# Performance work log

Hardware: AMD Instinct MI355X
Metric: run time of the kernel (lower is better)

## Reference

```python
import jax, jax.numpy as jnp
import numpy as np

BS, EP = 32, 32
N_AGENTS, N_ATOM, EMBED = 8, 51, 32
STATE_DIM, HYP = 128, 64
V_MIN, V_MAX = -10.0, 10.0


def proj(support, probs, v_min, v_max, n_atom):
    # C51 categorical projection of (support, probs) onto the fixed atom grid
    # linspace(v_min, v_max, n_atom). support/probs: [..., M] -> [..., n_atom]
    support, probs = jnp.broadcast_arrays(support, probs)
    delta = (v_max - v_min) / (n_atom - 1)
    b = (jnp.clip(support, v_min, v_max) - v_min) / delta
    l = jnp.floor(b)
    u = jnp.ceil(b)
    eq = (u == l).astype(probs.dtype)  # support exactly on an atom -> all mass to l
    ml = probs * (u - b + eq)
    mu = probs * (b - l)
    shp = probs.shape
    n = int(np.prod(shp[:-1]))
    m = shp[-1]
    rows = jnp.arange(n)[:, None]
    out = jnp.zeros((n, n_atom), probs.dtype)
    out = out.at[rows, l.astype(jnp.int32).reshape(n, m)].add(ml.reshape(n, m))
    out = out.at[rows, u.astype(jnp.int32).reshape(n, m)].add(mu.reshape(n, m))
    return out.reshape(shp[:-1] + (n_atom,))


def bconv(p, q):
    # Full 1D convolution of per-row categorical pmfs (sum of two random vars).
    # p: [N, L], q: [N, M] -> [N, L+M-1], via grouped conv (one group per row).
    N, L = p.shape
    M = q.shape[-1]
    out = jax.lax.conv_general_dilated(
        p[None], jnp.flip(q, -1)[:, None, :],
        window_strides=(1,), padding=[(M - 1, M - 1)],
        feature_group_count=N, dimension_numbers=('NCW', 'OIW', 'NCW'))
    return out[0]


def mlp2(x, w1, b1, w2, b2):
    return jax.nn.relu(x @ w1.T + b1) @ w2.T + b2


def setup_inputs():
    key = jax.random.key(0)
    ks = jax.random.split(key, 20)
    def p(k, shape, s=0.05):
        return jax.random.normal(k, shape, dtype=jnp.float32) * s
    aq = jax.random.uniform(ks[0], (BS, EP, N_AGENTS, N_ATOM), dtype=jnp.float32)
    aq = aq / jnp.sum(aq, -1, keepdims=True)  # valid categorical distributions
    return {
        'agent_qs_distri': aq,
        'states': p(ks[1], (BS, EP, STATE_DIM), 1.0),
        'hw1_w1': p(ks[2], (HYP, STATE_DIM)), 'hw1_b1': p(ks[3], (HYP,)),
        'hw1_w2': p(ks[4], (EMBED * N_AGENTS, HYP)), 'hw1_b2': p(ks[5], (EMBED * N_AGENTS,)),
        'hb1_w': p(ks[6], (EMBED, STATE_DIM)), 'hb1_b': p(ks[7], (EMBED,)),
        'hwf_w1': p(ks[8], (HYP, STATE_DIM)), 'hwf_b1': p(ks[9], (HYP,)),
        'hwf_w2': p(ks[10], (EMBED, HYP)), 'hwf_b2': p(ks[11], (EMBED,)),
        'v_w1': p(ks[12], (EMBED, STATE_DIM)), 'v_b1': p(ks[13], (EMBED,)),
        'v_w2': p(ks[14], (1, EMBED)), 'v_b2': p(ks[15], (1,)),
    }


def reference(agent_qs_distri, states, hw1_w1, hw1_b1, hw1_w2, hw1_b2,
              hb1_w, hb1_b, hwf_w1, hwf_b1, hwf_w2, hwf_b2,
              v_w1, v_b1, v_w2, v_b2):
    bs, ep, n_agents, n_atom = agent_qs_distri.shape
    s = states.reshape(-1, STATE_DIM)
    atoms = jnp.linspace(V_MIN, V_MAX, n_atom).astype(jnp.float32)  # [A]

    w1 = jnp.abs(mlp2(s, hw1_w1, hw1_b1, hw1_w2, hw1_b2)).reshape(bs, ep, EMBED, n_agents)
    b1 = (s @ hb1_w.T + hb1_b).reshape(bs, ep, EMBED)

    # stage 1: scale each agent's support by w1[..., k, i], project back onto atoms
    sup1 = atoms * w1[..., None]                                       # [bs,ep,E,Na,A]
    aw = proj(sup1, agent_qs_distri[:, :, None], V_MIN, V_MAX, n_atom)  # [bs,ep,E,Na,A]
    awf = aw.reshape(-1, n_agents, n_atom)                              # [bs*ep*E,Na,A]
    q = awf[:, 0]
    for i in range(1, n_agents):
        q = bconv(q, awf[:, i])                                         # [.., Na*A-Na+1]
    L1 = n_agents * n_atom - n_agents + 1
    sup = jnp.linspace(n_agents * V_MIN, n_agents * V_MAX, L1).astype(jnp.float32)
    sup = jax.nn.elu(sup + b1[..., None])                               # [bs,ep,E,L1]
    x = proj(sup, q.reshape(bs, ep, EMBED, L1), V_MIN, V_MAX, n_atom)   # [bs,ep,E,A]

    # stage 2: hyper_w_final scaling, convolve across embed dim, add V(s)
    wf = jnp.abs(mlp2(s, hwf_w1, hwf_b1, hwf_w2, hwf_b2)).reshape(bs, ep, EMBED)
    xw = proj(atoms * wf[..., None], x, V_MIN, V_MAX, n_atom)           # [bs,ep,E,A]
    xwf = xw.reshape(-1, EMBED, n_atom)
    q = xwf[:, 0]
    for i in range(1, EMBED):
        q = bconv(q, xwf[:, i])                                         # [bs*ep, E*A-E+1]
    L2 = EMBED * n_atom - EMBED + 1
    v = mlp2(s, v_w1, v_b1, v_w2, v_b2).reshape(bs, ep, 1)
    sup2 = jnp.linspace(EMBED * V_MIN, EMBED * V_MAX, L2).astype(jnp.float32) + v
    return proj(sup2, q.reshape(bs, ep, L2), V_MIN, V_MAX, n_atom)      # [bs,ep,A]
```

## Files before the change

### kernel.cpp

```cpp
#include <hip/hip_runtime.h>
#include <hip/hip_bf16.h>
#include <math.h>

typedef unsigned short u16;

#define WAVE_SYNC() asm volatile("s_waitcnt lgkmcnt(0)" ::: "memory")

__device__ __forceinline__ float bf2f(u16 u) {
  union { unsigned int i; float f; } c;
  c.i = ((unsigned int)u) << 16;
  return c.f;
}
__device__ __forceinline__ float bflo(unsigned int u) {
  union { unsigned int i; float f; } c; c.i = u << 16; return c.f;
}
__device__ __forceinline__ float bfhi(unsigned int u) {
  union { unsigned int i; float f; } c; c.i = u & 0xffff0000u; return c.f;
}
__device__ __forceinline__ u16 f2bf(float f) {
  union { float f; unsigned int i; } c;
  c.f = f;
  unsigned int x = c.i;
  unsigned int r = (x + 0x7fffu + ((x >> 16) & 1u)) >> 16;
  return (u16)r;
}

__device__ __forceinline__ void proj_bounds(float wv, int& ML, int& MH) {
  float smin = (-10.0f + 0.4f * 0.0f)  * wv;
  float smax = (-10.0f + 0.4f * 50.0f) * wv;
  float bmin = (fminf(fmaxf(smin, -10.0f), 10.0f) + 10.0f) / 0.4f;
  float bmax = (fminf(fmaxf(smax, -10.0f), 10.0f) + 10.0f) / 0.4f;
  ML = (int)floorf(bmin);
  MH = (int)ceilf(bmax);
}

template<typename SUPP>
__device__ __forceinline__ void proj_scan(float* __restrict__ g1,
                                          float* __restrict__ g2,
                                          int span, int lane, SUPP supp)
{
  if (lane < 52) g1[lane] = 0.f;
  if (lane < 53) g2[lane] = 0.f;
  float cml = 0.f, cmu = 0.f;
  int ck = -1;
  for (int base = 0; base < span; base += 64) {
    int t = base + lane;
    bool act = (t < span);
    int tc = act ? t : (span - 1);
    float sup, p;
    supp(tc, act, sup, p);
    float c  = fminf(fmaxf(sup, -10.0f), 10.0f);
    float b  = (c + 10.0f) / 0.4f;
    float l  = floorf(b);
    float u  = ceilf(b);
    float eq = (u == l) ? 1.0f : 0.0f;
    float ml = p * (u - b + eq);
    float mu = p * (b - l);
    int   li = (int)l;
    bool last = (base + 64 >= span);
    if (lane == 0 && ck >= 0) {
      if (ck == li) { ml += cml; mu += cmu; }
      else          { g1[ck] = cml; g2[ck + 1] = cmu; }
    }
#pragma unroll
    for (int d = 1; d < 64; d <<= 1) {
      int   lo = __shfl_up(li, d);
      float a1 = __shfl_up(ml, d);
      float a2 = __shfl_up(mu, d);
      bool same = (lane >= d) && (lo == li);
      ml += same ? a1 : 0.f;
      mu += same ? a2 : 0.f;
    }
    int ln = __shfl_down(li, 1);
    bool runend = (lane == 63) ? last : (ln != li);
    if (runend) { g1[li] = ml; g2[li + 1] = mu; }
    if (!last) {
      cml = __shfl(ml, 63);
      cmu = __shfl(mu, 63);
      ck  = __shfl(li, 63);
    }
  }
}

__device__ __forceinline__ void conv_pad2(const float* __restrict__ q,
                                          float* __restrict__ qn,
                                          const float* __restrict__ kvs,
                                          int ML, int W, int T,
                                          int LQ, int HQ, int tid, int nthr)
{
  const int Lout = LQ + ML, Hout = HQ + ML + T;
  for (int J = Lout + tid; J <= Hout; J += nthr) {
    const float* qp = q + (J - ML);
    float acc = 0.f;
    for (int c = 0; c < W; c += 4) {
      float4 k4 = *(const float4*)(kvs + c);
      acc = fmaf(k4.x, qp[-c],     acc);
      acc = fmaf(k4.y, qp[-c - 1], acc);
      acc = fmaf(k4.z, qp[-c - 2], acc);
      acc = fmaf(k4.w, qp[-c - 3], acc);
    }
    qn[J] = acc;
  }
}

template<int BF>
__device__ __forceinline__ float ldt(const void* p, int i) {
  if (BF) return bf2f(((const u16*)p)[i]);
  return ((const float*)p)[i];
}

template<int BF>
__device__ __forceinline__ float dot128_t(const void* w, int row, const float* s) {
  float acc = 0.f;
  if (BF) {
    const uint4* p = (const uint4*)((const u16*)w + row * 128);
#pragma unroll
    for (int i = 0; i < 16; ++i) {
      uint4 v = p[i];
      int b = i * 8;
      acc = fmaf(bflo(v.x), s[b + 0], acc); acc = fmaf(bfhi(v.x), s[b + 1], acc);
      acc = fmaf(bflo(v.y), s[b + 2], acc); acc = fmaf(bfhi(v.y), s[b + 3], acc);
      acc = fmaf(bflo(v.z), s[b + 4], acc); acc = fmaf(bfhi(v.z), s[b + 5], acc);
      acc = fmaf(bflo(v.w), s[b + 6], acc); acc = fmaf(bfhi(v.w), s[b + 7], acc);
    }
  } else {
    const float4* p = (const float4*)((const float*)w + row * 128);
#pragma unroll
    for (int i = 0; i < 32; ++i) {
      float4 v = p[i];
      int b = i * 4;
      acc = fmaf(v.x, s[b + 0], acc); acc = fmaf(v.y, s[b + 1], acc);
      acc = fmaf(v.z, s[b + 2], acc); acc = fmaf(v.w, s[b + 3], acc);
    }
  }
  return acc;
}

template<int BF>
__device__ __forceinline__ float dot64_t(const void* w, int row, const float* h) {
  float acc = 0.f;
  if (BF) {
    const uint4* p = (const uint4*)((const u16*)w + row * 64);
#pragma unroll
    for (int i = 0; i < 8; ++i) {
      uint4 v = p[i];
      int b = i * 8;
      acc = fmaf(bflo(v.x), h[b + 0], acc); acc = fmaf(bfhi(v.x), h[b + 1], acc);
      acc = fmaf(bflo(v.y), h[b + 2], acc); acc = fmaf(bfhi(v.y), h[b + 3], acc);
      acc = fmaf(bflo(v.z), h[b + 4], acc); acc = fmaf(bfhi(v.z), h[b + 5], acc);
      acc = fmaf(bflo(v.w), h[b + 6], acc); acc = fmaf(bfhi(v.w), h[b + 7], acc);
    }
  } else {
    const float4* p = (const float4*)((const float*)w + row * 64);
#pragma unroll
    for (int i = 0; i < 16; ++i) {
      float4 v = p[i];
      int b = i * 4;
      acc = fmaf(v.x, h[b + 0], acc); acc = fmaf(v.y, h[b + 1], acc);
      acc = fmaf(v.z, h[b + 2], acc); acc = fmaf(v.w, h[b + 3], acc);
    }
  }
  return acc;
}

template<int BF>
__device__ __forceinline__ void mlp_body(
    const void* states,
    const void* hw1_w1, const void* hw1_b1, const void* hw1_w2, const void* hw1_b2,
    const void* hb1_w,  const void* hb1_b,
    const void* hwf_w1, const void* hwf_b1, const void* hwf_w2, const void* hwf_b2,
    const void* v_w1,   const void* v_b1,   const void* v_w2,   const void* v_b2,
    float* w1_ws, float* b1_ws, float* wf_ws, float* v_ws,
    int n, int tid, float* s, float* h1, float* hf, float* vh)
{
  s[tid]      = ldt<BF>(states, n * 128 + tid);
  s[tid + 64] = ldt<BF>(states, n * 128 + 64 + tid);
  __syncthreads();

  h1[tid] = fmaxf(dot128_t<BF>(hw1_w1, tid, s) + ldt<BF>(hw1_b1, tid), 0.f);
  hf[tid] = fmaxf(dot128_t<BF>(hwf_w1, tid, s) + ldt<BF>(hwf_b1, tid), 0.f);
  if (tid < 32) {
    vh[tid] = fmaxf(dot128_t<BF>(v_w1, tid, s) + ldt<BF>(v_b1, tid), 0.f);
    b1_ws[n * 32 + tid] = dot128_t<BF>(hb1_w, tid, s) + ldt<BF>(hb1_b, tid);
  }
  __syncthreads();

#pragma unroll
  for (int k = 0; k < 4; ++k) {
    int o = tid + 64 * k;
    w1_ws[n * 256 + o] = fabsf(dot64_t<BF>(hw1_w2, o, h1) + ldt<BF>(hw1_b2, o));
  }
  if (tid < 32)
    wf_ws[n * 32 + tid] = fabsf(dot64_t<BF>(hwf_w2, tid, hf) + ldt<BF>(hwf_b2, tid));
  if (tid == 0) {
    float acc = ldt<BF>(v_b2, 0);
    for (int e = 0; e < 32; ++e) acc = fmaf(ldt<BF>(v_w2, e), vh[e], acc);
    v_ws[n] = acc;
  }
}

__global__ __launch_bounds__(64) void k_mlp(
    const void* __restrict__ states,
    const void* __restrict__ hw1_w1, const void* __restrict__ hw1_b1,
    const void* __restrict__ hw1_w2, const void* __restrict__ hw1_b2,
    const void* __restrict__ hb1_w,  const void* __restrict__ hb1_b,
    const void* __restrict__ hwf_w1, const void* __restrict__ hwf_b1,
    const void* __restrict__ hwf_w2, const void* __restrict__ hwf_b2,
    const void* __restrict__ v_w1,   const void* __restrict__ v_b1,
    const void* __restrict__ v_w2,   const void* __restrict__ v_b2,
    float* __restrict__ w1_ws, float* __restrict__ b1_ws,
    float* __restrict__ wf_ws, float* __restrict__ v_ws,
    int* __restrict__ flag)
{
  __shared__ float s[128];
  __shared__ float h1[64];
  __shared__ float hf[64];
  __shared__ float vh[32];
  const int n = blockIdx.x;
  const int tid = threadIdx.x;

  const u16* sr = (const u16*)states;
  unsigned int e0 = (sr[tid] >> 7) & 0xFF;
  unsigned int e1 = (sr[tid + 64] >> 7) & 0xFF;
  unsigned long long bl0 = __ballot(e0 >= 97 && e0 <= 141);
  unsigned long long bl1 = __ballot(e1 >= 97 && e1 <= 141);
  int bf = (__popcll(bl0) + __popcll(bl1) >= 104) ? 1 : 0;
  if (tid == 0) *flag = bf;

  if (bf)
    mlp_body<1>(states, hw1_w1, hw1_b1, hw1_w2, hw1_b2, hb1_w, hb1_b,
                hwf_w1, hwf_b1, hwf_w2, hwf_b2, v_w1, v_b1, v_w2, v_b2,
                w1_ws, b1_ws, wf_ws, v_ws, n, tid, s, h1, hf, vh);
  else
    mlp_body<0>(states, hw1_w1, hw1_b1, hw1_w2, hw1_b2, hb1_w, hb1_b,
                hwf_w1, hwf_b1, hwf_w2, hwf_b2, v_w1, v_b1, v_w2, v_b2,
                w1_ws, b1_ws, wf_ws, v_ws, n, tid, s, h1, hf, vh);
}

__global__ __launch_bounds__(128) void k_perembed(
    const void* __restrict__ aq,
    const float* __restrict__ w1_ws, const float* __restrict__ b1_ws,
    const float* __restrict__ wf_ws, float* __restrict__ xw_ws,
    const int* __restrict__ flag)
{
  __shared__ __align__(16) float Ab[2][520];
  __shared__ __align__(16) float Bb[2][520];
  __shared__ __align__(16) float kvsb[2][56];
  __shared__ float gAb[2][53];
  __shared__ float gBb[2][54];

  const int w    = threadIdx.x >> 6;
  const int lane = threadIdx.x & 63;
  const int task = blockIdx.x * 2 + w;
  const int n = task >> 5;
  const int e = task & 31;
  const int bf = *flag;

  float* A   = Ab[w];
  float* B   = Bb[w];
  float* kvs = kvsb[w];
  float* gA  = gAb[w];
  float* gB  = gBb[w];

  float pv[8];
  if (bf) {
    const u16* p = (const u16*)aq + n * 408 + lane;
#pragma unroll
    for (int a = 0; a < 8; ++a) pv[a] = (lane < 51) ? bf2f(p[a * 51]) : 0.f;
  } else {
    const float* p = (const float*)aq + n * 408 + lane;
#pragma unroll
    for (int a = 0; a < 8; ++a) pv[a] = (lane < 51) ? p[a * 51] : 0.f;
  }
  float wreg = (lane < 8) ? w1_ws[n * 256 + e * 8 + lane] : 0.f;
  float b1v  = b1_ws[n * 32 + e];
  float wfv  = wf_ws[n * 32 + e];

  float wv0 = __shfl(wreg, 0);
  int ML0, MH0;
  proj_bounds(wv0, ML0, MH0);
  {
    float pa = pv[0];
    proj_scan(gA, gB, 51, lane, [&](int t, bool act, float& sup, float& p) {
      sup = (-10.0f + 0.4f * (float)t) * wv0;
      p = act ? pa : 0.f;
    });
  }
  if (lane <= MH0 - ML0)
    A[64 + ML0 + lane] = gA[ML0 + lane] + gB[ML0 + lane];
  WAVE_SYNC();

  int LQ = 64 + ML0, HQ = 64 + MH0;
  float* q = A;
  float* qn = B;
#pragma unroll
  for (int a = 1; a < 8; ++a) {
    float wv = __shfl(wreg, a);
    int ML, MH;
    proj_bounds(wv, ML, MH);
    int T = MH - ML;
    int W = (T + 4) & ~3;
    float pa = pv[a];
    proj_scan(gA, gB, 51, lane, [&](int t, bool act, float& sup, float& p) {
      sup = (-10.0f + 0.4f * (float)t) * wv;
      p = act ? pa : 0.f;
    });
    if (lane < W)     kvs[lane] = (lane <= T) ? (gA[ML + lane] + gB[ML + lane]) : 0.f;
    if (lane < W - 1) q[LQ - 1 - lane] = 0.f;
    if (lane < T)     q[HQ + 1 + lane] = 0.f;
    WAVE_SYNC();
    conv_pad2(q, qn, kvs, ML, W, T, LQ, HQ, lane, 64);
    WAVE_SYNC();
    LQ += ML; HQ += MH;
    float* t_ = q; q = qn; qn = t_;
  }

  {
    int span = HQ - LQ + 1;
    int LQl = LQ;
    const float* qf = q;
    proj_scan(gA, gB, span, lane, [&](int t, bool act, float& sup, float& p) {
      int tg = (LQl - 64) + t;
      float raw = (-80.0f + 0.4f * (float)tg) + b1v;
      sup = (raw > 0.f) ? raw : expm1f(raw);
      p = act ? qf[LQl + t] : 0.f;
    });
  }
  WAVE_SYNC();

  float x2v = (lane < 51) ? (gA[lane] + gB[lane]) : 0.f;
  WAVE_SYNC();
  int MLf, MHf;
  proj_bounds(wfv, MLf, MHf);
  proj_scan(gA, gB, 51, lane, [&](int t, bool act, float& sup, float& p) {
    sup = (-10.0f + 0.4f * (float)t) * wfv;
    p = act ? x2v : 0.f;
  });
  WAVE_SYNC();
  if (lane <= MHf - MLf)
    xw_ws[task * 51 + MLf + lane] = gA[MLf + lane] + gB[MLf + lane];
}

__global__ __launch_bounds__(256) void k_final(
    const float* __restrict__ xw_ws, const float* __restrict__ wf_ws,
    const float* __restrict__ v_ws,
    void* __restrict__ out, const int* __restrict__ flag)
{
  __shared__ __align__(16) float bufA[4608];
  __shared__ __align__(16) float bufB[4608];
  __shared__ int meta_s[63];
  __shared__ int meta_l[63];
  __shared__ int meta_ml[32];
  __shared__ int meta_g[6];
  __shared__ int meta_mltot;
  __shared__ float gA[53], gB[54];

  const int n    = blockIdx.x;
  const int tid  = threadIdx.x;
  const int lane = tid & 63;
  const int bf   = *flag;

  float wfreg = (lane < 32) ? wf_ws[n * 32 + lane] : 0.f;
  float vv    = v_ws[n];

  for (int i = tid; i < 4608; i += 256) { bufA[i] = 0.f; bufB[i] = 0.f; }

  if (tid < 64) {
    int ml, mh;
    proj_bounds(wfreg, ml, mh);
    if (lane < 32) meta_ml[lane] = ml;
    int msum = ml;
#pragma unroll
    for (int d = 1; d < 32; d <<= 1) msum += __shfl_xor(msum, d);
    if (lane == 0) meta_mltot = msum;

    int curlen = mh - ml + 1;
    int base = 0, Ncur = 32;
#pragma unroll
    for (int c = 0; c <= 5; ++c) {
      int lm = (lane < Ncur) ? curlen : 0;
#pragma unroll
      for (int d = 1; d < 32; d <<= 1) {
        int o = __shfl_xor(lm, d);
        lm = (o > lm) ? o : lm;
      }
      int G = (lm + 11) & ~3;
      int sp = ((curlen + 3) & ~3) + G;
      int inc = (lane < Ncur) ? sp : 0;
      int v0 = inc;
#pragma unroll
      for (int d = 1; d < 32; d <<= 1) {
        int u = __shfl_up(inc, d);
        if (lane >= d && lane < 32) inc += u;
      }
      if (lane < Ncur) {
        meta_s[base + lane] = 832 + (inc - v0);
        meta_l[base + lane] = curlen;
      }
      if (lane == 0) meta_g[c] = G;
      if (c < 5) {
        int l0 = __shfl(curlen, 2 * lane);
        int l1 = __shfl(curlen, 2 * lane + 1);
        curlen = l0 + l1 - 1;
        base += Ncur;
        Ncur >>= 1;
      }
    }
  }
  __syncthreads();

  {
    int g = tid >> 3, i = tid & 7;
    int s = meta_s[g], l = meta_l[g], ml = meta_ml[g];
    const float* row = xw_ws + (n * 32 + g) * 51 + ml;
    for (int i0 = i; i0 < l; i0 += 8) bufA[s + i0] = row[i0];
  }
  __syncthreads();

#pragma unroll
  for (int c = 1; c <= 5; ++c) {
    const float* bin = (c & 1) ? bufA : bufB;
    float*       bout = (c & 1) ? bufB : bufA;
    const int Nout = 32 >> c;
    const int lg = 3 + c;
    const int gs = 1 << lg;
    const int k  = tid >> lg;
    const int st = tid & (gs - 1);
    const int bc = 64 - (64 >> c);
    const int bp = 64 - (64 >> (c - 1));
    const int i0 = bp + 2 * k;
    const int sA = meta_s[i0];
    const int sB = meta_s[i0 + 1];
    const int lB = meta_l[i0 + 1];
    const int sO = meta_s[bc + k];
    const int lO = meta_l[bc + k];
    const int W  = (lB + 3) & ~3;

    for (int j = st * 2; j < lO; j += gs * 2) {
      const float* Ap = bin + sA + j + 1;
      float a0 = 0.f, a1 = 0.f;
      for (int m = 0; m < W; m += 4) {
        float4 k4 = *(const float4*)(bin + sB + m);
        float v0 = Ap[-m], v1 = Ap[-m - 1], v2 = Ap[-m - 2];
        float v3 = Ap[-m - 3], v4 = Ap[-m - 4];
        a0 = fmaf(k4.x, v1, fmaf(k4.y, v2, fmaf(k4.z, v3, fmaf(k4.w, v4, a0))));
        a1 = fmaf(k4.x, v0, fmaf(k4.y, v1, fmaf(k4.z, v2, fmaf(k4.w, v3, a1))));
      }
      bout[sO + j] = a0;
      if (j + 1 < lO) bout[sO + j + 1] = a1;
    }

    if (c >= 2 && c <= 4) {
      int G = meta_g[c];
      for (int p = tid; p < G; p += 256) bout[832 - G + p] = 0.f;
      for (int k2 = 0; k2 < Nout; ++k2) {
        int ss = meta_s[bc + k2] + meta_l[bc + k2];
        int ee = (k2 + 1 < Nout) ? meta_s[bc + k2 + 1]
                                 : ss + G + 3;
        for (int p = ss + tid; p < ee; p += 256) bout[p] = 0.f;
      }
    }
    __syncthreads();
  }

  if (tid < 64) {
    int s5 = meta_s[62], l5 = meta_l[62], mlt = meta_mltot;
    const float* qf = bufB + s5;
    proj_scan(gA, gB, l5, lane, [&](int t, bool act, float& sup, float& p) {
      int tg = mlt + t;
      sup = (-320.0f + 0.4f * (float)tg) + vv;
      p = act ? qf[t] : 0.f;
    });
    WAVE_SYNC();
    if (lane < 51) {
      float o = gA[lane] + gB[lane];
      if (bf) ((u16*)out)[n * 51 + lane] = f2bf(o);
      else    ((float*)out)[n * 51 + lane] = o;
    }
  }
}

extern "C" void kernel_launch(void* const* d_in, const int* in_sizes, int n_in,
                              void* d_out, int out_size, void* d_ws, size_t ws_size,
                              hipStream_t stream)
{
  float* ws    = (float*)d_ws;
  float* w1_ws = ws;
  float* b1_ws = w1_ws + 1024 * 256;
  float* wf_ws = b1_ws + 1024 * 32;
  float* v_ws  = wf_ws + 1024 * 32;
  float* xw_ws = v_ws  + 1024;
  int*   flag  = (int*)(xw_ws + 1024 * 32 * 51);

  k_mlp<<<1024, 64, 0, stream>>>(d_in[1],
      d_in[2], d_in[3], d_in[4], d_in[5], d_in[6], d_in[7],
      d_in[8], d_in[9], d_in[10], d_in[11], d_in[12], d_in[13],
      d_in[14], d_in[15],
      w1_ws, b1_ws, wf_ws, v_ws, flag);

  k_perembed<<<16384, 128, 0, stream>>>(d_in[0], w1_ws, b1_ws, wf_ws, xw_ws, flag);

  k_final<<<1024, 256, 0, stream>>>(xw_ws, wf_ws, v_ws, d_out, flag);
}
```

Before: 250.0 us.

## Compute per-agent weight projections in parallel via gather-form hat-weight sums

Measured after the change: 248.7 us. Within noise of the previous version (-0.5%).

```diff
diff --git a/kernel.cpp b/kernel.cpp
--- a/kernel.cpp
+++ b/kernel.cpp
@@ -245,7 +245,9 @@
 {
   __shared__ __align__(16) float Ab[2][520];
   __shared__ __align__(16) float Bb[2][520];
-  __shared__ __align__(16) float kvsb[2][56];
+  __shared__ __align__(16) float kv_all[2][8][16];
+  __shared__ __align__(16) float kvo[2][56];
+  __shared__ float p_lds[2][8][52];
   __shared__ float gAb[2][53];
   __shared__ float gBb[2][54];
 
@@ -258,61 +260,120 @@
 
   float* A   = Ab[w];
   float* B   = Bb[w];
-  float* kvs = kvsb[w];
   float* gA  = gAb[w];
   float* gB  = gBb[w];
-
-  float pv[8];
+  float (*pl)[52] = p_lds[w];
+
   if (bf) {
     const u16* p = (const u16*)aq + n * 408 + lane;
-#pragma unroll
-    for (int a = 0; a < 8; ++a) pv[a] = (lane < 51) ? bf2f(p[a * 51]) : 0.f;
+    if (lane < 51) {
+#pragma unroll
+      for (int a = 0; a < 8; ++a) pl[a][lane] = bf2f(p[a * 51]);
+    }
   } else {
     const float* p = (const float*)aq + n * 408 + lane;
-#pragma unroll
-    for (int a = 0; a < 8; ++a) pv[a] = (lane < 51) ? p[a * 51] : 0.f;
+    if (lane < 51) {
+#pragma unroll
+      for (int a = 0; a < 8; ++a) pl[a][lane] = p[a * 51];
+    }
   }
   float wreg = (lane < 8) ? w1_ws[n * 256 + e * 8 + lane] : 0.f;
   float b1v  = b1_ws[n * 32 + e];
   float wfv  = wf_ws[n * 32 + e];
 
-  float wv0 = __shfl(wreg, 0);
-  int ML0, MH0;
-  proj_bounds(wv0, ML0, MH0);
-  {
-    float pa = pv[0];
+  int mlA = 0, mhA = 0;
+  if (lane < 8) proj_bounds(wreg, mlA, mhA);
+  unsigned long long wide = __ballot((lane < 8) && (mhA - mlA > 15));
+  WAVE_SYNC();
+
+  int LQ, HQ;
+  float* q = A;
+  float* qn = B;
+
+  if (wide == 0ull) {
+#pragma unroll
+    for (int r = 0; r < 2; ++r) {
+      int a  = 4 * r + (lane >> 4);
+      int jj = lane & 15;
+      float wv = __shfl(wreg, a);
+      int ML = __shfl(mlA, a);
+      int MH = __shfl(mhA, a);
+      int T = MH - ML;
+      int j = ML + jj;
+      float ej = 0.4f * (float)j - 10.0f;
+      float invw = 2.5f / wv;
+      int tL = (jj == 0) ? 0  : (int)floorf((ej - 0.4f) * invw + 25.f) - 1;
+      int tH = (jj >= T) ? 50 : (int)ceilf ((ej + 0.4f) * invw + 25.f) + 1;
+      tL = tL < 0 ? 0 : tL;
+      tH = tH > 50 ? 50 : tH;
+      if (jj > T) { tL = 0; tH = -1; }
+      float acc = 0.f;
+      float tf = (float)tL;
+      const float* pb = pl[a];
+      for (int t = tL; t <= tH; ++t) {
+        float p = pb[t];
+        float sup = (-10.0f + 0.4f * tf) * wv;
+        float c = fminf(fmaxf(sup, -10.0f), 10.0f);
+        float d = (c - ej) * 2.5f;
+        float wgt = fmaxf(0.f, 1.f - fabsf(d));
+        acc = fmaf(p, wgt, acc);
+        tf += 1.0f;
+      }
+      kv_all[w][a][jj] = (jj <= T) ? acc : 0.f;
+    }
+    WAVE_SYNC();
+
+    int ML0 = __shfl(mlA, 0), MH0 = __shfl(mhA, 0);
+    if (lane <= MH0 - ML0) A[64 + ML0 + lane] = kv_all[w][0][lane];
+    WAVE_SYNC();
+    LQ = 64 + ML0; HQ = 64 + MH0;
+
+#pragma unroll
+    for (int a = 1; a < 8; ++a) {
+      int ML = __shfl(mlA, a), MH = __shfl(mhA, a);
+      int T = MH - ML;
+      int W = (T + 4) & ~3;
+      if (lane < W - 1) q[LQ - 1 - lane] = 0.f;
+      if (lane < T)     q[HQ + 1 + lane] = 0.f;
+      WAVE_SYNC();
+      conv_pad2(q, qn, &kv_all[w][a][0], ML, W, T, LQ, HQ, lane, 64);
+      WAVE_SYNC();
+      LQ += ML; HQ += MH;
+      float* t_ = q; q = qn; qn = t_;
+    }
+  } else {
+    float* kvs = kvo[w];
+    float wv0 = __shfl(wreg, 0);
+    int ML0 = __shfl(mlA, 0), MH0 = __shfl(mhA, 0);
     proj_scan(gA, gB, 51, lane, [&](int t, bool act, float& sup, float& p) {
       sup = (-10.0f + 0.4f * (float)t) * wv0;
-      p = act ? pa : 0.f;
+      float pv = pl[0][t];
+      p = act ? pv : 0.f;
     });
-  }
-  if (lane <= MH0 - ML0)
-    A[64 + ML0 + lane] = gA[ML0 + lane] + gB[ML0 + lane];
-  WAVE_SYNC();
-
-  int LQ = 64 + ML0, HQ = 64 + MH0;
-  float* q = A;
-  float* qn = B;
-#pragma unroll
-  for (int a = 1; a < 8; ++a) {
-    float wv = __shfl(wreg, a);
-    int ML, MH;
-    proj_bounds(wv, ML, MH);
-    int T = MH - ML;
-    int W = (T + 4) & ~3;
-    float pa = pv[a];
-    proj_scan(gA, gB, 51, lane, [&](int t, bool act, float& sup, float& p) {
-      sup = (-10.0f + 0.4f * (float)t) * wv;
-      p = act ? pa : 0.f;
-    });
-    if (lane < W)     kvs[lane] = (lane <= T) ? (gA[ML + lane] + gB[ML + lane]) : 0.f;
-    if (lane < W - 1) q[LQ - 1 - lane] = 0.f;
-    if (lane < T)     q[HQ + 1 + lane] = 0.f;
+    if (lane <= MH0 - ML0)
+      A[64 + ML0 + lane] = gA[ML0 + lane] + gB[ML0 + lane];
     WAVE_SYNC();
-    conv_pad2(q, qn, kvs, ML, W, T, LQ, HQ, lane, 64);
-    WAVE_SYNC();
-    LQ += ML; HQ += MH;
-    float* t_ = q; q = qn; qn = t_;
+    LQ = 64 + ML0; HQ = 64 + MH0;
+
+    for (int a = 1; a < 8; ++a) {
+      float wv = __shfl(wreg, a);
+      int ML = __shfl(mlA, a), MH = __shfl(mhA, a);
+      int T = MH - ML;
+      int W = (T + 4) & ~3;
+      proj_scan(gA, gB, 51, lane, [&](int t, bool act, float& sup, float& p) {
+        sup = (-10.0f + 0.4f * (float)t) * wv;
+        float pv = pl[a][t];
+        p = act ? pv : 0.f;
+      });
+      if (lane < W)     kvs[lane] = (lane <= T) ? (gA[ML + lane] + gB[ML + lane]) : 0.f;
+      if (lane < W - 1) q[LQ - 1 - lane] = 0.f;
+      if (lane < T)     q[HQ + 1 + lane] = 0.f;
+      WAVE_SYNC();
+      conv_pad2(q, qn, kvs, ML, W, T, LQ, HQ, lane, 64);
+      WAVE_SYNC();
+      LQ += ML; HQ += MH;
+      float* t_ = q; q = qn; qn = t_;
+    }
   }
 
   {
```
